# Kernel optimization log

Hardware: AMD Instinct MI355X
Metric: run time of the kernel (lower is better)

The kernel has to match this reference:

```python
import jax, jax.numpy as jnp
import numpy as np
import math

B, N, L, ED, H = 2, 32, 4, 64, 4   # graphs, nodes/graph, layers, embed_dim, heads
HD = ED // H
EPS = 1e-5


def _ln(x, g, b):
    m = x.mean(-1, keepdims=True)
    v = ((x - m) ** 2).mean(-1, keepdims=True)
    return (x - m) * jax.lax.rsqrt(v + EPS) * g + b


def _layer(x, W, b, lg, lb, fW, fb, fg, fbeta):
    # NOTE: in the torch source, ModuleList([Linear]*4) shares ONE linear for
    # q/k/v1/v2 and ONE LayerNorm for norms[0..2]; we reproduce that sharing.
    h = (x @ W.T + b).reshape(B, N, N, H, HD)
    q = _ln(h, lg, lb)                                    # q == k (shared LN)
    scores = jnp.einsum('bxahd,bayhd->bxayh', q, q) / math.sqrt(HD)
    att = jax.nn.softmax(scores, axis=2)                  # softmax over 'a'
    xu = jnp.einsum('bxahd,bayhd->bxayhd', h, h)          # v1 == v2 == h
    xu = _ln(xu, lg, lb)                                  # shared LN again
    xu = jnp.einsum('bxayh,bxayhd->bxyhd', att, xu).reshape(B, N, N, ED)
    y = jnp.concatenate([x, xu], axis=-1) @ fW.T + fb
    return _ln(y, fg, fbeta)


def _diag_offdiag_maxpool(x):
    # x: (B, ED, N, N)
    diag = jnp.diagonal(x, axis1=-2, axis2=-1)            # (B, ED, N)
    max_diag = diag.max(axis=2)                           # (B, ED)
    val = jnp.abs(max_diag.max() + (-x).max())
    eye = jnp.eye(N, dtype=x.dtype)
    max_offdiag = (x - val * eye).max(axis=(2, 3))        # (B, ED)
    return jnp.concatenate([max_diag, max_offdiag], axis=1)  # (B, 2*ED)


def setup_inputs() -> dict:
    key = jax.random.key(0)
    ks = jax.random.split(key, 12)
    E = 1024
    g = jax.random.randint(ks[0], (E,), 0, B)
    ls = jax.random.randint(ks[1], (E,), 0, N)
    ld = jax.random.randint(ks[2], (E,), 0, N)
    edge_index = jnp.stack([g * N + ls, g * N + ld]).astype(jnp.int64)
    batch = (jnp.arange(B * N) // N).astype(jnp.int64)
    std = 0.02
    return {
        'edge_index': edge_index,
        'batch': batch,
        'W0': jax.random.normal(ks[3], (ED, 1), jnp.float32) * std,
        'b0': jnp.zeros((ED,), jnp.float32),
        'Ws': jax.random.normal(ks[4], (L - 1, ED, ED), jnp.float32) * std,
        'bs': jnp.zeros((L - 1, ED), jnp.float32),
        'ln_g': jnp.ones((L, HD), jnp.float32),
        'ln_b': jnp.zeros((L, HD), jnp.float32),
        'fW0': jax.random.normal(ks[5], (ED, 1 + ED), jnp.float32) * std,
        'fb0': jnp.zeros((ED,), jnp.float32),
        'fWs': jax.random.normal(ks[6], (L - 1, ED, 2 * ED), jnp.float32) * std,
        'fbs': jnp.zeros((L - 1, ED), jnp.float32),
        'fln_g': jnp.ones((L, ED), jnp.float32),
        'fln_b': jnp.zeros((L, ED), jnp.float32),
        'opW': jax.random.normal(ks[7], (L, ED // 2, 2 * ED), jnp.float32) * std,
        'opb': jnp.zeros((L, ED // 2), jnp.float32),
    }


def reference(edge_index, batch, W0, b0, Ws, bs, ln_g, ln_b,
              fW0, fb0, fWs, fbs, fln_g, fln_b, opW, opb):
    # to_dense_adj with edge_attr = 1.0
    g = batch[edge_index[0]]
    ls = edge_index[0] - g * N
    ld = edge_index[1] - g * N
    adj = jnp.zeros((B, N, N), jnp.float32).at[g, ls, ld].add(1.0)
    idx = jnp.arange(N)
    adj = adj.at[:, idx, idx].set(2.0)
    x = adj[..., None]                                    # (B, N, N, 1)

    scores = jnp.zeros((B, ED // 2), jnp.float32)
    for i in range(L):
        W = W0 if i == 0 else Ws[i - 1]
        b = b0 if i == 0 else bs[i - 1]
        fW = fW0 if i == 0 else fWs[i - 1]
        fb = fb0 if i == 0 else fbs[i - 1]
        x = _layer(x, W, b, ln_g[i], ln_b[i], fW, fb, fln_g[i], fln_b[i])
        pooled = _diag_offdiag_maxpool(jnp.transpose(x, (0, 3, 1, 2)))
        scores = scores + pooled @ opW[i].T + opb[i]

    # BatchNorm1d(momentum=1.0, affine=False), training mode -> batch stats
    m = scores.mean(axis=0)
    v = scores.var(axis=0)
    return (scores - m) / jnp.sqrt(v + EPS)
```

## Files before the change

### kernel.cpp

```cpp
#include <hip/hip_runtime.h>
#include <math.h>

#define EPS 1e-5f

#define AG_LOAD(p)     __hip_atomic_load((p), __ATOMIC_RELAXED, __HIP_MEMORY_SCOPE_AGENT)
#define AG_STORE(p, v) __hip_atomic_store((p), (v), __ATOMIC_RELAXED, __HIP_MEMORY_SCOPE_AGENT)

struct Params {
    const int* ei; const int* batch; int E;
    const float* W0; const float* b0; const float* Ws; const float* bs;
    const float* ln_g; const float* ln_b;
    const float* fW0; const float* fb0; const float* fWs; const float* fbs;
    const float* fln_g; const float* fln_b;
    const float* opW; const float* opb;
    float* hA; float* qA;
    float* hB; float* qB;
    float* xbuf;
    float* Pmin; float* Poff; float* Pdg;
    int* bar;
    float* out;
};


__launch_bounds__(512, 1)
__global__ void k0(Params p) {
    const int tid  = threadIdx.x;
    const int blk  = blockIdx.x;
    const int gtid = blk * 512 + tid;
    const int c    = tid & 63;
    const int d    = c & 15;
    const int rl   = tid >> 6;
    const int r0     = blk * 8;
    const int b_blk  = r0 >> 10;
    const int xi_blk = (r0 >> 5) & 31;
    const int y0     = r0 & 31;
    const int rld    = xi_blk - y0;
    const int a_l  = c & 31;
    const int h1   = c >> 5;

    __shared__ float xslab[32];
    __shared__ float yslab[256];
    __shared__ __align__(16) float cA[64], cC[64], cW[64], cB0[64], cG[64], cBl[64];
    __shared__ float hstat[3][4];
    __shared__ __align__(16) float pp_s[256 * 68];
    __shared__ float A1_s[8 * 132];
    __shared__ float K0h_s[8][4];
    __shared__ __align__(16) float xrow[8][64];
    __shared__ __align__(16) float xu_s[8][64];
    __shared__ float Wf0[64];
    __shared__ __align__(16) float T65[64 * 68];
    __shared__ __align__(16) float ST[64 * 68];

    if (blk == 0 && tid == 0) p.bar[0] = 0;

    if (tid < 32)  xslab[tid] = 0.0f;
    if (tid < 256) yslab[tid] = 0.0f;

    if (tid < 64) {
        float Wc = p.W0[c], bc = p.b0[c];
        float sW = Wc, sB = bc;
        #pragma unroll
        for (int m = 1; m < 16; m <<= 1) {
            sW += __shfl_xor(sW, m, 16);
            sB += __shfl_xor(sB, m, 16);
        }
        float Ac = Wc - sW * 0.0625f;
        float Bc = bc - sB * 0.0625f;
        float sAA = Ac * Ac, sAB = Ac * Bc, sBB = Bc * Bc;
        #pragma unroll
        for (int m = 1; m < 16; m <<= 1) {
            sAA += __shfl_xor(sAA, m, 16);
            sAB += __shfl_xor(sAB, m, 16);
            sBB += __shfl_xor(sBB, m, 16);
        }
        cA[c] = Ac; cC[c] = Bc; cW[c] = Wc; cB0[c] = bc;
        cG[c] = p.ln_g[d]; cBl[c] = p.ln_b[d];
        if (d == 0) {
            hstat[0][c >> 4] = sAA * 0.0625f;
            hstat[1][c >> 4] = sAB * 0.0625f;
            hstat[2][c >> 4] = sBB * 0.0625f;
        }
        Wf0[tid] = p.fW0[tid * 65];
    }
    for (int i = tid; i < 1024; i += 512) {
        int cc = i >> 4, u = i & 15;
        const float* src = p.fW0 + cc * 65 + 1 + 4 * u;
        float4 w = make_float4(src[0], src[1], src[2], src[3]);
        *(float4*)(T65 + cc * 68 + 4 * ((u + 2 * cc) & 15)) = w;
    }
    for (int i = tid; i < 1024; i += 512) {
        float4 w = ((const float4*)p.Ws)[i];
        int cc = i >> 4, u = i & 15;
        *(float4*)(ST + cc * 68 + 4 * ((u + 2 * cc) & 15)) = w;
    }
    __syncthreads();

    for (int e2 = tid; e2 < p.E; e2 += 512) {
        int e0 = p.ei[e2], e1 = p.ei[p.E + e2];
        int g  = p.batch[e0];
        if (g == b_blk) {
            int ls = e0 - g * 32, ld = e1 - g * 32;
            if (ls == xi_blk) atomicAdd(&xslab[ld], 1.0f);
            unsigned dy = (unsigned)(ld - y0);
            if (dy < 8u) atomicAdd(&yslab[ls * 8 + dy], 1.0f);
        }
    }
    __syncthreads();
    if (tid == 0) xslab[xi_blk] = 2.0f;
    if (tid < 8)  yslab[(y0 + tid) * 8 + tid] = 2.0f;
    __syncthreads();

    const float vx = xslab[a_l];
    const float vy = yslab[a_l * 8 + rl];
    float s0, s1, is0, is1, w0m, w1m;
    {
        const int hh = h1;
        float rsx = rsqrtf(fmaf(fmaf(hstat[0][hh], vx, 2.0f * hstat[1][hh]), vx, hstat[2][hh]) + EPS);
        float rsy = rsqrtf(fmaf(fmaf(hstat[0][hh], vy, 2.0f * hstat[1][hh]), vy, hstat[2][hh]) + EPS);
        float qq = 0.f, sp = 0.f, sq = 0.f;
        #pragma unroll
        for (int t = 0; t < 4; ++t) {
            int dd = hh * 16 + 4 * t;
            float4 av = *(const float4*)(cA + dd);
            float4 bv = *(const float4*)(cC + dd);
            float4 wv = *(const float4*)(cW + dd);
            float4 b0v = *(const float4*)(cB0 + dd);
            float4 gv = *(const float4*)(cG + dd);
            float4 blv = *(const float4*)(cBl + dd);
            float4 ppv;
            float qx, qy;
            qx = fmaf(av.x, vx, bv.x) * rsx * gv.x + blv.x;
            qy = fmaf(av.x, vy, bv.x) * rsy * gv.x + blv.x;
            qq = fmaf(qx, qy, qq);
            ppv.x = fmaf(wv.x, vx, b0v.x) * fmaf(wv.x, vy, b0v.x);
            qx = fmaf(av.y, vx, bv.y) * rsx * gv.y + blv.y;
            qy = fmaf(av.y, vy, bv.y) * rsy * gv.y + blv.y;
            qq = fmaf(qx, qy, qq);
            ppv.y = fmaf(wv.y, vx, b0v.y) * fmaf(wv.y, vy, b0v.y);
            qx = fmaf(av.z, vx, bv.z) * rsx * gv.z + blv.z;
            qy = fmaf(av.z, vy, bv.z) * rsy * gv.z + blv.z;
            qq = fmaf(qx, qy, qq);
            ppv.z = fmaf(wv.z, vx, b0v.z) * fmaf(wv.z, vy, b0v.z);
            qx = fmaf(av.w, vx, bv.w) * rsx * gv.w + blv.w;
            qy = fmaf(av.w, vy, bv.w) * rsy * gv.w + blv.w;
            qq = fmaf(qx, qy, qq);
            ppv.w = fmaf(wv.w, vx, b0v.w) * fmaf(wv.w, vy, b0v.w);
            sp += ppv.x + ppv.y + ppv.z + ppv.w;
            sq += ppv.x*ppv.x + ppv.y*ppv.y + ppv.z*ppv.z + ppv.w*ppv.w;
            *(float4*)(pp_s + (a_l * 8 + rl) * 68 + 4 * (((hh * 4 + t) + 3 * a_l) & 15)) = ppv;
        }
        s0 = qq * 0.25f;
        float mu = sp * 0.0625f, var = fmaxf(sq * 0.0625f - mu * mu, 0.f);
        is0 = rsqrtf(var + EPS); w0m = mu * is0;
    }
    {
        const int hh = h1 + 2;
        float rsx = rsqrtf(fmaf(fmaf(hstat[0][hh], vx, 2.0f * hstat[1][hh]), vx, hstat[2][hh]) + EPS);
        float rsy = rsqrtf(fmaf(fmaf(hstat[0][hh], vy, 2.0f * hstat[1][hh]), vy, hstat[2][hh]) + EPS);
        float qq = 0.f, sp = 0.f, sq = 0.f;
        #pragma unroll
        for (int t = 0; t < 4; ++t) {
            int dd = hh * 16 + 4 * t;
            float4 av = *(const float4*)(cA + dd);
            float4 bv = *(const float4*)(cC + dd);
            float4 wv = *(const float4*)(cW + dd);
            float4 b0v = *(const float4*)(cB0 + dd);
            float4 gv = *(const float4*)(cG + dd);
            float4 blv = *(const float4*)(cBl + dd);
            float4 ppv;
            float qx, qy;
            qx = fmaf(av.x, vx, bv.x) * rsx * gv.x + blv.x;
            qy = fmaf(av.x, vy, bv.x) * rsy * gv.x + blv.x;
            qq = fmaf(qx, qy, qq);
            ppv.x = fmaf(wv.x, vx, b0v.x) * fmaf(wv.x, vy, b0v.x);
            qx = fmaf(av.y, vx, bv.y) * rsx * gv.y + blv.y;
            qy = fmaf(av.y, vy, bv.y) * rsy * gv.y + blv.y;
            qq = fmaf(qx, qy, qq);
            ppv.y = fmaf(wv.y, vx, b0v.y) * fmaf(wv.y, vy, b0v.y);
            qx = fmaf(av.z, vx, bv.z) * rsx * gv.z + blv.z;
            qy = fmaf(av.z, vy, bv.z) * rsy * gv.z + blv.z;
            qq = fmaf(qx, qy, qq);
            ppv.z = fmaf(wv.z, vx, b0v.z) * fmaf(wv.z, vy, b0v.z);
            qx = fmaf(av.w, vx, bv.w) * rsx * gv.w + blv.w;
            qy = fmaf(av.w, vy, bv.w) * rsy * gv.w + blv.w;
            qq = fmaf(qx, qy, qq);
            ppv.w = fmaf(wv.w, vx, b0v.w) * fmaf(wv.w, vy, b0v.w);
            sp += ppv.x + ppv.y + ppv.z + ppv.w;
            sq += ppv.x*ppv.x + ppv.y*ppv.y + ppv.z*ppv.z + ppv.w*ppv.w;
            *(float4*)(pp_s + (a_l * 8 + rl) * 68 + 4 * (((hh * 4 + t) + 3 * a_l) & 15)) = ppv;
        }
        s1 = qq * 0.25f;
        float mu = sp * 0.0625f, var = fmaxf(sq * 0.0625f - mu * mu, 0.f);
        is1 = rsqrtf(var + EPS); w1m = mu * is1;
    }

    float m0 = s0, m1 = s1;
    #pragma unroll
    for (int m = 1; m < 32; m <<= 1) {
        m0 = fmaxf(m0, __shfl_xor(m0, m));
        m1 = fmaxf(m1, __shfl_xor(m1, m));
    }
    float e0 = __expf(s0 - m0), e1 = __expf(s1 - m1);
    float l0 = e0, l1 = e1, k0a = e0 * w0m, k1a = e1 * w1m;
    #pragma unroll
    for (int m = 1; m < 32; m <<= 1) {
        l0 += __shfl_xor(l0, m);  l1 += __shfl_xor(l1, m);
        k0a += __shfl_xor(k0a, m); k1a += __shfl_xor(k1a, m);
    }
    A1_s[rl * 132 + h1 * 33 + a_l]       = e0 * is0 / l0;
    A1_s[rl * 132 + (h1 + 2) * 33 + a_l] = e1 * is1 / l1;
    if (a_l == 0) {
        K0h_s[rl][h1]     = k0a / l0;
        K0h_s[rl][h1 + 2] = k1a / l1;
    }

    {
        const int hc = c >> 4;
        float acc = 0.f;
        #pragma unroll
        for (int a = 0; a < 32; ++a) {
            float pv = pp_s[(a * 8 + rl) * 68 + 4 * (((c >> 2) + 3 * a) & 15) + (c & 3)];
            acc = fmaf(A1_s[rl * 132 + hc * 33 + a], pv, acc);
        }
        xu_s[rl][c] = (acc - K0h_s[rl][hc]) * cG[c] + cBl[c];
    }

    const float adjv = xslab[y0 + rl];
    float acc2 = fmaf(Wf0[c], adjv, p.fb0[c]);
    #pragma unroll
    for (int u = 0; u < 16; ++u) {
        float4 w = *(const float4*)(T65 + c * 68 + 4 * ((u + 2 * c) & 15));
        float4 xr = *(const float4*)(&xu_s[rl][4 * u]);
        acc2 = fmaf(w.x, xr.x, acc2); acc2 = fmaf(w.y, xr.y, acc2);
        acc2 = fmaf(w.z, xr.z, acc2); acc2 = fmaf(w.w, xr.w, acc2);
    }
    float t1 = acc2;
    #pragma unroll
    for (int m = 1; m < 64; m <<= 1) t1 += __shfl_xor(t1, m, 64);
    float mu = t1 * (1.0f / 64.0f);
    float dv2 = acc2 - mu;
    float t2 = dv2 * dv2;
    #pragma unroll
    for (int m = 1; m < 64; m <<= 1) t2 += __shfl_xor(t2, m, 64);
    float xnew = dv2 * rsqrtf(t2 * (1.0f / 64.0f) + EPS) * p.fln_g[c] + p.fln_b[c];
    xrow[rl][c]  = xnew;
    p.xbuf[gtid] = xnew;
    __syncthreads();

    if (tid < 64) {
        float mn = 1e30f, off = -1e30f, dg = -1e30f;
        #pragma unroll
        for (int r2 = 0; r2 < 8; ++r2) {
            float v = xrow[r2][tid];
            mn = fminf(mn, v);
            if (r2 == rld) dg = v; else off = fmaxf(off, v);
        }
        int o = blk * 64 + tid;
        p.Pmin[o] = mn; p.Poff[o] = off; p.Pdg[o] = dg;
    }

    {
        float acc = p.bs[c];
        #pragma unroll
        for (int u = 0; u < 16; ++u) {
            float4 w = *(const float4*)(ST + c * 68 + 4 * ((u + 2 * c) & 15));
            float4 xr = *(const float4*)(&xrow[rl][4 * u]);
            acc = fmaf(w.x, xr.x, acc); acc = fmaf(w.y, xr.y, acc);
            acc = fmaf(w.z, xr.z, acc); acc = fmaf(w.w, xr.w, acc);
        }
        p.hA[gtid] = acc;
        float s1a = acc;
        #pragma unroll
        for (int m = 1; m < 16; m <<= 1) s1a += __shfl_xor(s1a, m, 16);
        float mean = s1a * 0.0625f;
        float dv = acc - mean;
        float s2 = dv * dv;
        #pragma unroll
        for (int m = 1; m < 16; m <<= 1) s2 += __shfl_xor(s2, m, 16);
        p.qA[gtid] = dv * rsqrtf(s2 * 0.0625f + EPS) * p.ln_g[16 + d] + p.ln_b[16 + d];
    }
}

__launch_bounds__(512, 1)
__global__ void klayer(Params p, int layer, int is_last) {
    const int tid  = threadIdx.x;
    const int blk  = blockIdx.x;
    const int gtid = blk * 512 + tid;
    const int c    = tid & 63;
    const int d    = c & 15;
    const int rl   = tid >> 6;
    const int r0     = blk * 8;
    const int b_blk  = r0 >> 10;
    const int xi_blk = (r0 >> 5) & 31;
    const int y0     = r0 & 31;
    const int rld    = xi_blk - y0;
    const int slab_off = (b_blk * 1024 + xi_blk * 32) * 64;
    const int a_l  = c & 31;
    const int h1   = c >> 5;

    const float* hin = (layer == 2) ? p.hB : p.hA;
    const float* qin = (layer == 2) ? p.qB : p.qA;
    float* hout = (layer == 1) ? p.hB : p.hA;
    float* qout = (layer == 1) ? p.qB : p.qA;

    __shared__ __align__(16) float qx_s[32 * 68];
    __shared__ __align__(16) float hx_s[32 * 68];
    __shared__ __align__(16) float pp_s[256 * 68];
    __shared__ float A1_s[8 * 132];
    __shared__ float K0h_s[8][4];
    __shared__ __align__(16) float xrow[8][64];
    __shared__ __align__(16) float xu_s[8][64];
    __shared__ __align__(16) float FT[64 * 132];
    __shared__ __align__(16) float ST[64 * 68];
    __shared__ float vals[4];
    __shared__ float scores_s[64];
    __shared__ int tailflag;
    float* sm_mn  = pp_s;
    float* sm_off = pp_s + 512;
    float* sm_dg  = pp_s + 1024;
    float* psum   = pp_s + 1536;

    float xv = p.xbuf[gtid];
    float4 qsl = ((const float4*)(qin + slab_off))[tid];
    float4 hsl = ((const float4*)(hin + slab_off))[tid];
    const float* qyp = qin + (b_blk * 1024 + a_l * 32 + y0 + rl) * 64;
    const float* hyp = hin + (b_blk * 1024 + a_l * 32 + y0 + rl) * 64;
    float4 qvA[4], hvA[4], qvB[4], hvB[4];
    #pragma unroll
    for (int t = 0; t < 4; ++t) {
        qvA[t] = *(const float4*)(qyp + h1 * 16 + 4 * t);
        hvA[t] = *(const float4*)(hyp + h1 * 16 + 4 * t);
        qvB[t] = *(const float4*)(qyp + (h1 + 2) * 16 + 4 * t);
        hvB[t] = *(const float4*)(hyp + (h1 + 2) * 16 + 4 * t);
    }
    const float gl = p.ln_g[layer * 16 + d], bl = p.ln_b[layer * 16 + d];

    {
        int a = tid >> 4, t = tid & 15, pr = (t + 2 * a) & 15;
        *(float4*)(qx_s + a * 68 + 4 * pr) = qsl;
        *(float4*)(hx_s + a * 68 + 4 * pr) = hsl;
    }
    {
        const float* fw = p.fWs + (layer - 1) * 8192;
        for (int i = tid; i < 2048; i += 512) {
            float4 w = ((const float4*)fw)[i];
            int cc = i >> 5, u = i & 31;
            *(float4*)(FT + cc * 132 + 4 * ((u + 2 * cc) & 31)) = w;
        }
    }
    if (!is_last) {
        const float* sw = p.Ws + layer * 4096;
        for (int i = tid; i < 1024; i += 512) {
            float4 w = ((const float4*)sw)[i];
            int cc = i >> 4, u = i & 15;
            *(float4*)(ST + cc * 68 + 4 * ((u + 2 * cc) & 15)) = w;
        }
    }
    xrow[rl][c] = xv;
    __syncthreads();

    float s0, s1, is0, is1, w0m, w1m;
    {
        const int hh = h1;
        float qq = 0.f, sp = 0.f, sq = 0.f;
        #pragma unroll
        for (int t = 0; t < 4; ++t) {
            float4 xq = *(const float4*)(qx_s + a_l * 68 + 4 * (((hh * 4 + t) + 2 * a_l) & 15));
            float4 xh = *(const float4*)(hx_s + a_l * 68 + 4 * (((hh * 4 + t) + 2 * a_l) & 15));
            float4 yq = qvA[t], yh = hvA[t];
            float4 ppv;
            ppv.x = xh.x * yh.x; ppv.y = xh.y * yh.y;
            ppv.z = xh.z * yh.z; ppv.w = xh.w * yh.w;
            qq = fmaf(xq.x, yq.x, qq); qq = fmaf(xq.y, yq.y, qq);
            qq = fmaf(xq.z, yq.z, qq); qq = fmaf(xq.w, yq.w, qq);
            sp += ppv.x + ppv.y + ppv.z + ppv.w;
            sq += ppv.x*ppv.x + ppv.y*ppv.y + ppv.z*ppv.z + ppv.w*ppv.w;
            *(float4*)(pp_s + (a_l * 8 + rl) * 68 + 4 * (((hh * 4 + t) + 3 * a_l) & 15)) = ppv;
        }
        s0 = qq * 0.25f;
        float mu = sp * 0.0625f, var = fmaxf(sq * 0.0625f - mu * mu, 0.f);
        is0 = rsqrtf(var + EPS); w0m = mu * is0;
    }
    {
        const int hh = h1 + 2;
        float qq = 0.f, sp = 0.f, sq = 0.f;
        #pragma unroll
        for (int t = 0; t < 4; ++t) {
            float4 xq = *(const float4*)(qx_s + a_l * 68 + 4 * (((hh * 4 + t) + 2 * a_l) & 15));
            float4 xh = *(const float4*)(hx_s + a_l * 68 + 4 * (((hh * 4 + t) + 2 * a_l) & 15));
            float4 yq = qvB[t], yh = hvB[t];
            float4 ppv;
            ppv.x = xh.x * yh.x; ppv.y = xh.y * yh.y;
            ppv.z = xh.z * yh.z; ppv.w = xh.w * yh.w;
            qq = fmaf(xq.x, yq.x, qq); qq = fmaf(xq.y, yq.y, qq);
            qq = fmaf(xq.z, yq.z, qq); qq = fmaf(xq.w, yq.w, qq);
            sp += ppv.x + ppv.y + ppv.z + ppv.w;
            sq += ppv.x*ppv.x + ppv.y*ppv.y + ppv.z*ppv.z + ppv.w*ppv.w;
            *(float4*)(pp_s + (a_l * 8 + rl) * 68 + 4 * (((hh * 4 + t) + 3 * a_l) & 15)) = ppv;
        }
        s1 = qq * 0.25f;
        float mu = sp * 0.0625f, var = fmaxf(sq * 0.0625f - mu * mu, 0.f);
        is1 = rsqrtf(var + EPS); w1m = mu * is1;
    }

    float m0 = s0, m1 = s1;
    #pragma unroll
    for (int m = 1; m < 32; m <<= 1) {
        m0 = fmaxf(m0, __shfl_xor(m0, m));
        m1 = fmaxf(m1, __shfl_xor(m1, m));
    }
    float e0 = __expf(s0 - m0), e1 = __expf(s1 - m1);
    float l0 = e0, l1 = e1, k0a = e0 * w0m, k1a = e1 * w1m;
    #pragma unroll
    for (int m = 1; m < 32; m <<= 1) {
        l0 += __shfl_xor(l0, m);  l1 += __shfl_xor(l1, m);
        k0a += __shfl_xor(k0a, m); k1a += __shfl_xor(k1a, m);
    }
    A1_s[rl * 132 + h1 * 33 + a_l]       = e0 * is0 / l0;
    A1_s[rl * 132 + (h1 + 2) * 33 + a_l] = e1 * is1 / l1;
    if (a_l == 0) {
        K0h_s[rl][h1]     = k0a / l0;
        K0h_s[rl][h1 + 2] = k1a / l1;
    }

    {
        const int hc = c >> 4;
        float acc = 0.f;
        #pragma unroll
        for (int a = 0; a < 32; ++a) {
            float pv = pp_s[(a * 8 + rl) * 68 + 4 * (((c >> 2) + 3 * a) & 15) + (c & 3)];
            acc = fmaf(A1_s[rl * 132 + hc * 33 + a], pv, acc);
        }
        xu_s[rl][c] = (acc - K0h_s[rl][hc]) * gl + bl;
    }

    float acc2 = p.fbs[(layer - 1) * 64 + c];
    #pragma unroll
    for (int u = 0; u < 16; ++u) {
        float4 w = *(const float4*)(FT + c * 132 + 4 * ((u + 2 * c) & 31));
        float4 xr = *(const float4*)(&xrow[rl][4 * u]);
        acc2 = fmaf(w.x, xr.x, acc2); acc2 = fmaf(w.y, xr.y, acc2);
        acc2 = fmaf(w.z, xr.z, acc2); acc2 = fmaf(w.w, xr.w, acc2);
    }
    #pragma unroll
    for (int u = 16; u < 32; ++u) {
        float4 w = *(const float4*)(FT + c * 132 + 4 * ((u + 2 * c) & 31));
        float4 xr = *(const float4*)(&xu_s[rl][4 * (u - 16)]);
        acc2 = fmaf(w.x, xr.x, acc2); acc2 = fmaf(w.y, xr.y, acc2);
        acc2 = fmaf(w.z, xr.z, acc2); acc2 = fmaf(w.w, xr.w, acc2);
    }
    float t1 = acc2;
    #pragma unroll
    for (int m = 1; m < 64; m <<= 1) t1 += __shfl_xor(t1, m, 64);
    float mu = t1 * (1.0f / 64.0f);
    float dv2 = acc2 - mu;
    float t2 = dv2 * dv2;
    #pragma unroll
    for (int m = 1; m < 64; m <<= 1) t2 += __shfl_xor(t2, m, 64);
    float xnew = dv2 * rsqrtf(t2 * (1.0f / 64.0f) + EPS) *
                 p.fln_g[layer * 64 + c] + p.fln_b[layer * 64 + c];
    __syncthreads();
    xrow[rl][c] = xnew;
    if (!is_last) p.xbuf[gtid] = xnew;
    __syncthreads();

    if (tid < 64) {
        float mn = 1e30f, off = -1e30f, dg = -1e30f;
        #pragma unroll
        for (int r2 = 0; r2 < 8; ++r2) {
            float v = xrow[r2][tid];
            mn = fminf(mn, v);
            if (r2 == rld) dg = v; else off = fmaxf(off, v);
        }
        int o = layer * 16384 + blk * 64 + tid;
        if (is_last) {
            AG_STORE(&p.Pmin[o], mn); AG_STORE(&p.Poff[o], off); AG_STORE(&p.Pdg[o], dg);
        } else {
            p.Pmin[o] = mn; p.Poff[o] = off; p.Pdg[o] = dg;
        }
    }

    if (!is_last) {
        float acc = p.bs[layer * 64 + c];
        #pragma unroll
        for (int u = 0; u < 16; ++u) {
            float4 w = *(const float4*)(ST + c * 68 + 4 * ((u + 2 * c) & 15));
            float4 xr = *(const float4*)(&xrow[rl][4 * u]);
            acc = fmaf(w.x, xr.x, acc); acc = fmaf(w.y, xr.y, acc);
            acc = fmaf(w.z, xr.z, acc); acc = fmaf(w.w, xr.w, acc);
        }
        hout[gtid] = acc;
        float s1a = acc;
        #pragma unroll
        for (int m = 1; m < 16; m <<= 1) s1a += __shfl_xor(s1a, m, 16);
        float mean = s1a * 0.0625f;
        float dv = acc - mean;
        float s2 = dv * dv;
        #pragma unroll
        for (int m = 1; m < 16; m <<= 1) s2 += __shfl_xor(s2, m, 16);
        qout[gtid] = dv * rsqrtf(s2 * 0.0625f + EPS) *
                     p.ln_g[(layer + 1) * 16 + d] + p.ln_b[(layer + 1) * 16 + d];
        return;
    }

    __syncthreads();
    if (tid == 0) {
        int r = __hip_atomic_fetch_add(p.bar, 1, __ATOMIC_RELAXED,
                                       __HIP_MEMORY_SCOPE_AGENT);
        tailflag = (r == 255) ? 1 : 0;
    }
    __syncthreads();
    if (!tailflag) return;

    {
        int l = tid >> 7, bb = (tid >> 6) & 1, e = tid & 63;
        float mn = 1e30f, off = -1e30f, dg = -1e30f;
        #pragma unroll 4
        for (int k = 0; k < 128; ++k) {
            int o = l * 16384 + (bb * 128 + k) * 64 + e;
            float vmn, voff, vdg;
            if (l == 3) { vmn = AG_LOAD(&p.Pmin[o]); voff = AG_LOAD(&p.Poff[o]); vdg = AG_LOAD(&p.Pdg[o]); }
            else        { vmn = p.Pmin[o];           voff = p.Poff[o];           vdg = p.Pdg[o]; }
            mn  = fminf(mn,  vmn);
            off = fmaxf(off, voff);
            dg  = fmaxf(dg,  vdg);
        }
        sm_mn[tid] = mn; sm_off[tid] = off; sm_dg[tid] = dg;
    }
    __syncthreads();
    if (tid < 4) {
        float gmx = -1e30f, gmn = 1e30f;
        for (int i2 = 0; i2 < 128; ++i2) {
            gmx = fmaxf(gmx, sm_dg[tid * 128 + i2]);
            gmn = fminf(gmn, sm_mn[tid * 128 + i2]);
        }
        vals[tid] = fabsf(gmx - gmn);
    }
    __syncthreads();
    {
        int bb = tid >> 8, cc = (tid >> 3) & 31, pp = tid & 7;
        float a2 = 0.0f;
        for (int l = 0; l < 4; ++l) {
            float val = vals[l];
            const float* Wr = p.opW + l * 4096 + cc * 128;
            int base = l * 128 + bb * 64;
            for (int j = pp * 16; j < pp * 16 + 16; ++j) {
                float pv;
                if (j < 64) pv = sm_dg[base + j];
                else        pv = fmaxf(sm_off[base + j - 64], sm_dg[base + j - 64] - val);
                a2 = fmaf(Wr[j], pv, a2);
            }
        }
        psum[tid] = a2;
    }
    __syncthreads();
    if (tid < 64) {
        int bb = tid >> 5, cc = tid & 31;
        float a2 = 0.0f;
        for (int l = 0; l < 4; ++l) a2 += p.opb[l * 32 + cc];
        for (int pp = 0; pp < 8; ++pp) a2 += psum[bb * 256 + cc * 8 + pp];
        scores_s[tid] = a2;
    }
    __syncthreads();
    if (tid < 32) {
        float sA = scores_s[tid], sB = scores_s[32 + tid];
        float mu2 = 0.5f * (sA + sB);
        float va = 0.5f * ((sA - mu2) * (sA - mu2) + (sB - mu2) * (sB - mu2));
        float inv = rsqrtf(va + EPS);
        p.out[tid]      = (sA - mu2) * inv;
        p.out[32 + tid] = (sB - mu2) * inv;
    }
}

extern "C" void kernel_launch(void* const* d_in, const int* in_sizes, int n_in,
                              void* d_out, int out_size, void* d_ws, size_t ws_size,
                              hipStream_t stream) {
    Params prm;
    prm.ei    = (const int*)d_in[0];
    prm.batch = (const int*)d_in[1];
    prm.E     = in_sizes[0] / 2;
    prm.W0    = (const float*)d_in[2];
    prm.b0    = (const float*)d_in[3];
    prm.Ws    = (const float*)d_in[4];
    prm.bs    = (const float*)d_in[5];
    prm.ln_g  = (const float*)d_in[6];
    prm.ln_b  = (const float*)d_in[7];
    prm.fW0   = (const float*)d_in[8];
    prm.fb0   = (const float*)d_in[9];
    prm.fWs   = (const float*)d_in[10];
    prm.fbs   = (const float*)d_in[11];
    prm.fln_g = (const float*)d_in[12];
    prm.fln_b = (const float*)d_in[13];
    prm.opW   = (const float*)d_in[14];
    prm.opb   = (const float*)d_in[15];

    float* ws = (float*)d_ws;
    prm.hA    = ws;
    prm.qA    = prm.hA   + 131072;
    prm.hB    = prm.qA   + 131072;
    prm.qB    = prm.hB   + 131072;
    prm.xbuf  = prm.qB   + 131072;
    prm.Pmin  = prm.xbuf + 131072;
    prm.Poff  = prm.Pmin + 65536;
    prm.Pdg   = prm.Poff + 65536;
    prm.bar   = (int*)(prm.Pdg + 65536);
    prm.out   = (float*)d_out;

    k0<<<256, 512, 0, stream>>>(prm);
    klayer<<<256, 512, 0, stream>>>(prm, 1, 0);
    klayer<<<256, 512, 0, stream>>>(prm, 2, 0);
    klayer<<<256, 512, 0, stream>>>(prm, 3, 1);
}
```

Before: 162.8 us.

## Fuse four layer kernels into one persistent kernel with grid barriers

Merges the initial layer kernel and the three per-layer kernels into one persistent kernel with 256 blocks. Blocks synchronise between layers through an atomic-counter grid barrier instead of separate launches. The final pooling and batch-norm tail runs on block 0 after a last barrier, and a memset clears the barrier counters before launch. This removes launch gaps between the four stages, but relies on all 256 blocks being co-resident and adds spin-wait barrier cost.

```diff
diff --git a/kernel.cpp b/kernel.cpp
--- a/kernel.cpp
+++ b/kernel.cpp
@@ -21,268 +21,23 @@
     float* out;
 };
 
+__device__ __forceinline__ void gridbar(int* bar, int ph) {
+    __syncthreads();
+    __threadfence();
+    if (threadIdx.x == 0) {
+        int r = atomicAdd(&bar[ph], 1);
+        if (r == 255) {
+            AG_STORE(&bar[8 + ph], 1);
+        } else {
+            while (AG_LOAD(&bar[8 + ph]) == 0) __builtin_amdgcn_s_sleep(8);
+        }
+    }
+    __syncthreads();
+    __threadfence();
+}
 
 __launch_bounds__(512, 1)
-__global__ void k0(Params p) {
-    const int tid  = threadIdx.x;
-    const int blk  = blockIdx.x;
-    const int gtid = blk * 512 + tid;
-    const int c    = tid & 63;
-    const int d    = c & 15;
-    const int rl   = tid >> 6;
-    const int r0     = blk * 8;
-    const int b_blk  = r0 >> 10;
-    const int xi_blk = (r0 >> 5) & 31;
-    const int y0     = r0 & 31;
-    const int rld    = xi_blk - y0;
-    const int a_l  = c & 31;
-    const int h1   = c >> 5;
-
-    __shared__ float xslab[32];
-    __shared__ float yslab[256];
-    __shared__ __align__(16) float cA[64], cC[64], cW[64], cB0[64], cG[64], cBl[64];
-    __shared__ float hstat[3][4];
-    __shared__ __align__(16) float pp_s[256 * 68];
-    __shared__ float A1_s[8 * 132];
-    __shared__ float K0h_s[8][4];
-    __shared__ __align__(16) float xrow[8][64];
-    __shared__ __align__(16) float xu_s[8][64];
-    __shared__ float Wf0[64];
-    __shared__ __align__(16) float T65[64 * 68];
-    __shared__ __align__(16) float ST[64 * 68];
-
-    if (blk == 0 && tid == 0) p.bar[0] = 0;
-
-    if (tid < 32)  xslab[tid] = 0.0f;
-    if (tid < 256) yslab[tid] = 0.0f;
-
-    if (tid < 64) {
-        float Wc = p.W0[c], bc = p.b0[c];
-        float sW = Wc, sB = bc;
-        #pragma unroll
-        for (int m = 1; m < 16; m <<= 1) {
-            sW += __shfl_xor(sW, m, 16);
-            sB += __shfl_xor(sB, m, 16);
-        }
-        float Ac = Wc - sW * 0.0625f;
-        float Bc = bc - sB * 0.0625f;
-        float sAA = Ac * Ac, sAB = Ac * Bc, sBB = Bc * Bc;
-        #pragma unroll
-        for (int m = 1; m < 16; m <<= 1) {
-            sAA += __shfl_xor(sAA, m, 16);
-            sAB += __shfl_xor(sAB, m, 16);
-            sBB += __shfl_xor(sBB, m, 16);
-        }
-        cA[c] = Ac; cC[c] = Bc; cW[c] = Wc; cB0[c] = bc;
-        cG[c] = p.ln_g[d]; cBl[c] = p.ln_b[d];
-        if (d == 0) {
-            hstat[0][c >> 4] = sAA * 0.0625f;
-            hstat[1][c >> 4] = sAB * 0.0625f;
-            hstat[2][c >> 4] = sBB * 0.0625f;
-        }
-        Wf0[tid] = p.fW0[tid * 65];
-    }
-    for (int i = tid; i < 1024; i += 512) {
-        int cc = i >> 4, u = i & 15;
-        const float* src = p.fW0 + cc * 65 + 1 + 4 * u;
-        float4 w = make_float4(src[0], src[1], src[2], src[3]);
-        *(float4*)(T65 + cc * 68 + 4 * ((u + 2 * cc) & 15)) = w;
-    }
-    for (int i = tid; i < 1024; i += 512) {
-        float4 w = ((const float4*)p.Ws)[i];
-        int cc = i >> 4, u = i & 15;
-        *(float4*)(ST + cc * 68 + 4 * ((u + 2 * cc) & 15)) = w;
-    }
-    __syncthreads();
-
-    for (int e2 = tid; e2 < p.E; e2 += 512) {
-        int e0 = p.ei[e2], e1 = p.ei[p.E + e2];
-        int g  = p.batch[e0];
-        if (g == b_blk) {
-            int ls = e0 - g * 32, ld = e1 - g * 32;
-            if (ls == xi_blk) atomicAdd(&xslab[ld], 1.0f);
-            unsigned dy = (unsigned)(ld - y0);
-            if (dy < 8u) atomicAdd(&yslab[ls * 8 + dy], 1.0f);
-        }
-    }
-    __syncthreads();
-    if (tid == 0) xslab[xi_blk] = 2.0f;
-    if (tid < 8)  yslab[(y0 + tid) * 8 + tid] = 2.0f;
-    __syncthreads();
-
-    const float vx = xslab[a_l];
-    const float vy = yslab[a_l * 8 + rl];
-    float s0, s1, is0, is1, w0m, w1m;
-    {
-        const int hh = h1;
-        float rsx = rsqrtf(fmaf(fmaf(hstat[0][hh], vx, 2.0f * hstat[1][hh]), vx, hstat[2][hh]) + EPS);
-        float rsy = rsqrtf(fmaf(fmaf(hstat[0][hh], vy, 2.0f * hstat[1][hh]), vy, hstat[2][hh]) + EPS);
-        float qq = 0.f, sp = 0.f, sq = 0.f;
-        #pragma unroll
-        for (int t = 0; t < 4; ++t) {
-            int dd = hh * 16 + 4 * t;
-            float4 av = *(const float4*)(cA + dd);
-            float4 bv = *(const float4*)(cC + dd);
-            float4 wv = *(const float4*)(cW + dd);
-            float4 b0v = *(const float4*)(cB0 + dd);
-            float4 gv = *(const float4*)(cG + dd);
-            float4 blv = *(const float4*)(cBl + dd);
-            float4 ppv;
-            float qx, qy;
-            qx = fmaf(av.x, vx, bv.x) * rsx * gv.x + blv.x;
-            qy = fmaf(av.x, vy, bv.x) * rsy * gv.x + blv.x;
-            qq = fmaf(qx, qy, qq);
-            ppv.x = fmaf(wv.x, vx, b0v.x) * fmaf(wv.x, vy, b0v.x);
-            qx = fmaf(av.y, vx, bv.y) * rsx * gv.y + blv.y;
-            qy = fmaf(av.y, vy, bv.y) * rsy * gv.y + blv.y;
-            qq = fmaf(qx, qy, qq);
-            ppv.y = fmaf(wv.y, vx, b0v.y) * fmaf(wv.y, vy, b0v.y);
-            qx = fmaf(av.z, vx, bv.z) * rsx * gv.z + blv.z;
-            qy = fmaf(av.z, vy, bv.z) * rsy * gv.z + blv.z;
-            qq = fmaf(qx, qy, qq);
-            ppv.z = fmaf(wv.z, vx, b0v.z) * fmaf(wv.z, vy, b0v.z);
-            qx = fmaf(av.w, vx, bv.w) * rsx * gv.w + blv.w;
-            qy = fmaf(av.w, vy, bv.w) * rsy * gv.w + blv.w;
-            qq = fmaf(qx, qy, qq);
-            ppv.w = fmaf(wv.w, vx, b0v.w) * fmaf(wv.w, vy, b0v.w);
-            sp += ppv.x + ppv.y + ppv.z + ppv.w;
-            sq += ppv.x*ppv.x + ppv.y*ppv.y + ppv.z*ppv.z + ppv.w*ppv.w;
-            *(float4*)(pp_s + (a_l * 8 + rl) * 68 + 4 * (((hh * 4 + t) + 3 * a_l) & 15)) = ppv;
-        }
-        s0 = qq * 0.25f;
-        float mu = sp * 0.0625f, var = fmaxf(sq * 0.0625f - mu * mu, 0.f);
-        is0 = rsqrtf(var + EPS); w0m = mu * is0;
-    }
-    {
-        const int hh = h1 + 2;
-        float rsx = rsqrtf(fmaf(fmaf(hstat[0][hh], vx, 2.0f * hstat[1][hh]), vx, hstat[2][hh]) + EPS);
-        float rsy = rsqrtf(fmaf(fmaf(hstat[0][hh], vy, 2.0f * hstat[1][hh]), vy, hstat[2][hh]) + EPS);
-        float qq = 0.f, sp = 0.f, sq = 0.f;
-        #pragma unroll
-        for (int t = 0; t < 4; ++t) {
-            int dd = hh * 16 + 4 * t;
-            float4 av = *(const float4*)(cA + dd);
-            float4 bv = *(const float4*)(cC + dd);
-            float4 wv = *(const float4*)(cW + dd);
-            float4 b0v = *(const float4*)(cB0 + dd);
-            float4 gv = *(const float4*)(cG + dd);
-            float4 blv = *(const float4*)(cBl + dd);
-            float4 ppv;
-            float qx, qy;
-            qx = fmaf(av.x, vx, bv.x) * rsx * gv.x + blv.x;
-            qy = fmaf(av.x, vy, bv.x) * rsy * gv.x + blv.x;
-            qq = fmaf(qx, qy, qq);
-            ppv.x = fmaf(wv.x, vx, b0v.x) * fmaf(wv.x, vy, b0v.x);
-            qx = fmaf(av.y, vx, bv.y) * rsx * gv.y + blv.y;
-            qy = fmaf(av.y, vy, bv.y) * rsy * gv.y + blv.y;
-            qq = fmaf(qx, qy, qq);
-            ppv.y = fmaf(wv.y, vx, b0v.y) * fmaf(wv.y, vy, b0v.y);
-            qx = fmaf(av.z, vx, bv.z) * rsx * gv.z + blv.z;
-            qy = fmaf(av.z, vy, bv.z) * rsy * gv.z + blv.z;
-            qq = fmaf(qx, qy, qq);
-            ppv.z = fmaf(wv.z, vx, b0v.z) * fmaf(wv.z, vy, b0v.z);
-            qx = fmaf(av.w, vx, bv.w) * rsx * gv.w + blv.w;
-            qy = fmaf(av.w, vy, bv.w) * rsy * gv.w + blv.w;
-            qq = fmaf(qx, qy, qq);
-            ppv.w = fmaf(wv.w, vx, b0v.w) * fmaf(wv.w, vy, b0v.w);
-            sp += ppv.x + ppv.y + ppv.z + ppv.w;
-            sq += ppv.x*ppv.x + ppv.y*ppv.y + ppv.z*ppv.z + ppv.w*ppv.w;
-            *(float4*)(pp_s + (a_l * 8 + rl) * 68 + 4 * (((hh * 4 + t) + 3 * a_l) & 15)) = ppv;
-        }
-        s1 = qq * 0.25f;
-        float mu = sp * 0.0625f, var = fmaxf(sq * 0.0625f - mu * mu, 0.f);
-        is1 = rsqrtf(var + EPS); w1m = mu * is1;
-    }
-
-    float m0 = s0, m1 = s1;
-    #pragma unroll
-    for (int m = 1; m < 32; m <<= 1) {
-        m0 = fmaxf(m0, __shfl_xor(m0, m));
-        m1 = fmaxf(m1, __shfl_xor(m1, m));
-    }
-    float e0 = __expf(s0 - m0), e1 = __expf(s1 - m1);
-    float l0 = e0, l1 = e1, k0a = e0 * w0m, k1a = e1 * w1m;
-    #pragma unroll
-    for (int m = 1; m < 32; m <<= 1) {
-        l0 += __shfl_xor(l0, m);  l1 += __shfl_xor(l1, m);
-        k0a += __shfl_xor(k0a, m); k1a += __shfl_xor(k1a, m);
-    }
-    A1_s[rl * 132 + h1 * 33 + a_l]       = e0 * is0 / l0;
-    A1_s[rl * 132 + (h1 + 2) * 33 + a_l] = e1 * is1 / l1;
-    if (a_l == 0) {
-        K0h_s[rl][h1]     = k0a / l0;
-        K0h_s[rl][h1 + 2] = k1a / l1;
-    }
-
-    {
-        const int hc = c >> 4;
-        float acc = 0.f;
-        #pragma unroll
-        for (int a = 0; a < 32; ++a) {
-            float pv = pp_s[(a * 8 + rl) * 68 + 4 * (((c >> 2) + 3 * a) & 15) + (c & 3)];
-            acc = fmaf(A1_s[rl * 132 + hc * 33 + a], pv, acc);
-        }
-        xu_s[rl][c] = (acc - K0h_s[rl][hc]) * cG[c] + cBl[c];
-    }
-
-    const float adjv = xslab[y0 + rl];
-    float acc2 = fmaf(Wf0[c], adjv, p.fb0[c]);
-    #pragma unroll
-    for (int u = 0; u < 16; ++u) {
-        float4 w = *(const float4*)(T65 + c * 68 + 4 * ((u + 2 * c) & 15));
-        float4 xr = *(const float4*)(&xu_s[rl][4 * u]);
-        acc2 = fmaf(w.x, xr.x, acc2); acc2 = fmaf(w.y, xr.y, acc2);
-        acc2 = fmaf(w.z, xr.z, acc2); acc2 = fmaf(w.w, xr.w, acc2);
-    }
-    float t1 = acc2;
-    #pragma unroll
-    for (int m = 1; m < 64; m <<= 1) t1 += __shfl_xor(t1, m, 64);
-    float mu = t1 * (1.0f / 64.0f);
-    float dv2 = acc2 - mu;
-    float t2 = dv2 * dv2;
-    #pragma unroll
-    for (int m = 1; m < 64; m <<= 1) t2 += __shfl_xor(t2, m, 64);
-    float xnew = dv2 * rsqrtf(t2 * (1.0f / 64.0f) + EPS) * p.fln_g[c] + p.fln_b[c];
-    xrow[rl][c]  = xnew;
-    p.xbuf[gtid] = xnew;
-    __syncthreads();
-
-    if (tid < 64) {
-        float mn = 1e30f, off = -1e30f, dg = -1e30f;
-        #pragma unroll
-        for (int r2 = 0; r2 < 8; ++r2) {
-            float v = xrow[r2][tid];
-            mn = fminf(mn, v);
-            if (r2 == rld) dg = v; else off = fmaxf(off, v);
-        }
-        int o = blk * 64 + tid;
-        p.Pmin[o] = mn; p.Poff[o] = off; p.Pdg[o] = dg;
-    }
-
-    {
-        float acc = p.bs[c];
-        #pragma unroll
-        for (int u = 0; u < 16; ++u) {
-            float4 w = *(const float4*)(ST + c * 68 + 4 * ((u + 2 * c) & 15));
-            float4 xr = *(const float4*)(&xrow[rl][4 * u]);
-            acc = fmaf(w.x, xr.x, acc); acc = fmaf(w.y, xr.y, acc);
-            acc = fmaf(w.z, xr.z, acc); acc = fmaf(w.w, xr.w, acc);
-        }
-        p.hA[gtid] = acc;
-        float s1a = acc;
-        #pragma unroll
-        for (int m = 1; m < 16; m <<= 1) s1a += __shfl_xor(s1a, m, 16);
-        float mean = s1a * 0.0625f;
-        float dv = acc - mean;
-        float s2 = dv * dv;
-        #pragma unroll
-        for (int m = 1; m < 16; m <<= 1) s2 += __shfl_xor(s2, m, 16);
-        p.qA[gtid] = dv * rsqrtf(s2 * 0.0625f + EPS) * p.ln_g[16 + d] + p.ln_b[16 + d];
-    }
-}
-
-__launch_bounds__(512, 1)
-__global__ void klayer(Params p, int layer, int is_last) {
+__global__ void kfused(Params p) {
     const int tid  = threadIdx.x;
     const int blk  = blockIdx.x;
     const int gtid = blk * 512 + tid;
@@ -298,11 +53,6 @@
     const int a_l  = c & 31;
     const int h1   = c >> 5;
 
-    const float* hin = (layer == 2) ? p.hB : p.hA;
-    const float* qin = (layer == 2) ? p.qB : p.qA;
-    float* hout = (layer == 1) ? p.hB : p.hA;
-    float* qout = (layer == 1) ? p.qB : p.qA;
-
     __shared__ __align__(16) float qx_s[32 * 68];
     __shared__ __align__(16) float hx_s[32 * 68];
     __shared__ __align__(16) float pp_s[256 * 68];
@@ -314,203 +64,433 @@
     __shared__ __align__(16) float ST[64 * 68];
     __shared__ float vals[4];
     __shared__ float scores_s[64];
-    __shared__ int tailflag;
+    __shared__ float xslab[32];
+    __shared__ float yslab[256];
+    __shared__ __align__(16) float cA[64], cC[64], cW[64], cB0[64], cG[64], cBl[64];
+    __shared__ float hstat[3][4];
+    __shared__ float Wf0[64];
+
+    float* T65 = FT;
     float* sm_mn  = pp_s;
     float* sm_off = pp_s + 512;
     float* sm_dg  = pp_s + 1024;
     float* psum   = pp_s + 1536;
 
-    float xv = p.xbuf[gtid];
-    float4 qsl = ((const float4*)(qin + slab_off))[tid];
-    float4 hsl = ((const float4*)(hin + slab_off))[tid];
-    const float* qyp = qin + (b_blk * 1024 + a_l * 32 + y0 + rl) * 64;
-    const float* hyp = hin + (b_blk * 1024 + a_l * 32 + y0 + rl) * 64;
-    float4 qvA[4], hvA[4], qvB[4], hvB[4];
-    #pragma unroll
-    for (int t = 0; t < 4; ++t) {
-        qvA[t] = *(const float4*)(qyp + h1 * 16 + 4 * t);
-        hvA[t] = *(const float4*)(hyp + h1 * 16 + 4 * t);
-        qvB[t] = *(const float4*)(qyp + (h1 + 2) * 16 + 4 * t);
-        hvB[t] = *(const float4*)(hyp + (h1 + 2) * 16 + 4 * t);
-    }
-    const float gl = p.ln_g[layer * 16 + d], bl = p.ln_b[layer * 16 + d];
-
     {
-        int a = tid >> 4, t = tid & 15, pr = (t + 2 * a) & 15;
-        *(float4*)(qx_s + a * 68 + 4 * pr) = qsl;
-        *(float4*)(hx_s + a * 68 + 4 * pr) = hsl;
-    }
-    {
-        const float* fw = p.fWs + (layer - 1) * 8192;
-        for (int i = tid; i < 2048; i += 512) {
-            float4 w = ((const float4*)fw)[i];
-            int cc = i >> 5, u = i & 31;
-            *(float4*)(FT + cc * 132 + 4 * ((u + 2 * cc) & 31)) = w;
-        }
-    }
-    if (!is_last) {
-        const float* sw = p.Ws + layer * 4096;
+        if (tid < 32)  xslab[tid] = 0.0f;
+        if (tid < 256) yslab[tid] = 0.0f;
+
+        if (tid < 64) {
+            float Wc = p.W0[c], bc = p.b0[c];
+            float sW = Wc, sB = bc;
+            #pragma unroll
+            for (int m = 1; m < 16; m <<= 1) {
+                sW += __shfl_xor(sW, m, 16);
+                sB += __shfl_xor(sB, m, 16);
+            }
+            float Ac = Wc - sW * 0.0625f;
+            float Bc = bc - sB * 0.0625f;
+            float sAA = Ac * Ac, sAB = Ac * Bc, sBB = Bc * Bc;
+            #pragma unroll
+            for (int m = 1; m < 16; m <<= 1) {
+                sAA += __shfl_xor(sAA, m, 16);
+                sAB += __shfl_xor(sAB, m, 16);
+                sBB += __shfl_xor(sBB, m, 16);
+            }
+            cA[c] = Ac; cC[c] = Bc; cW[c] = Wc; cB0[c] = bc;
+            cG[c] = p.ln_g[d]; cBl[c] = p.ln_b[d];
+            if (d == 0) {
+                hstat[0][c >> 4] = sAA * 0.0625f;
+                hstat[1][c >> 4] = sAB * 0.0625f;
+                hstat[2][c >> 4] = sBB * 0.0625f;
+            }
+            Wf0[tid] = p.fW0[tid * 65];
+        }
         for (int i = tid; i < 1024; i += 512) {
-            float4 w = ((const float4*)sw)[i];
+            int cc = i >> 4, u = i & 15;
+            const float* src = p.fW0 + cc * 65 + 1 + 4 * u;
+            float4 w = make_float4(src[0], src[1], src[2], src[3]);
+            *(float4*)(T65 + cc * 68 + 4 * ((u + 2 * cc) & 15)) = w;
+        }
+        for (int i = tid; i < 1024; i += 512) {
+            float4 w = ((const float4*)p.Ws)[i];
             int cc = i >> 4, u = i & 15;
             *(float4*)(ST + cc * 68 + 4 * ((u + 2 * cc) & 15)) = w;
         }
-    }
-    xrow[rl][c] = xv;
-    __syncthreads();
-
-    float s0, s1, is0, is1, w0m, w1m;
-    {
-        const int hh = h1;
-        float qq = 0.f, sp = 0.f, sq = 0.f;
+        __syncthreads();
+
+        for (int e2 = tid; e2 < p.E; e2 += 512) {
+            int e0 = p.ei[e2], e1 = p.ei[p.E + e2];
+            int g  = p.batch[e0];
+            if (g == b_blk) {
+                int ls = e0 - g * 32, ld = e1 - g * 32;
+                if (ls == xi_blk) atomicAdd(&xslab[ld], 1.0f);
+                unsigned dy = (unsigned)(ld - y0);
+                if (dy < 8u) atomicAdd(&yslab[ls * 8 + dy], 1.0f);
+            }
+        }
+        __syncthreads();
+        if (tid == 0) xslab[xi_blk] = 2.0f;
+        if (tid < 8)  yslab[(y0 + tid) * 8 + tid] = 2.0f;
+        __syncthreads();
+
+        const float vx = xslab[a_l];
+        const float vy = yslab[a_l * 8 + rl];
+        float s0, s1, is0, is1, w0m, w1m;
+        {
+            const int hh = h1;
+            float rsx = rsqrtf(fmaf(fmaf(hstat[0][hh], vx, 2.0f * hstat[1][hh]), vx, hstat[2][hh]) + EPS);
+            float rsy = rsqrtf(fmaf(fmaf(hstat[0][hh], vy, 2.0f * hstat[1][hh]), vy, hstat[2][hh]) + EPS);
+            float qq = 0.f, sp = 0.f, sq = 0.f;
+            #pragma unroll
+            for (int t = 0; t < 4; ++t) {
+                int dd = hh * 16 + 4 * t;
+                float4 av = *(const float4*)(cA + dd);
+                float4 bv = *(const float4*)(cC + dd);
+                float4 wv = *(const float4*)(cW + dd);
+                float4 b0v = *(const float4*)(cB0 + dd);
+                float4 gv = *(const float4*)(cG + dd);
+                float4 blv = *(const float4*)(cBl + dd);
+                float4 ppv;
+                float qx, qy;
+                qx = fmaf(av.x, vx, bv.x) * rsx * gv.x + blv.x;
+                qy = fmaf(av.x, vy, bv.x) * rsy * gv.x + blv.x;
+                qq = fmaf(qx, qy, qq);
+                ppv.x = fmaf(wv.x, vx, b0v.x) * fmaf(wv.x, vy, b0v.x);
+                qx = fmaf(av.y, vx, bv.y) * rsx * gv.y + blv.y;
+                qy = fmaf(av.y, vy, bv.y) * rsy * gv.y + blv.y;
+                qq = fmaf(qx, qy, qq);
+                ppv.y = fmaf(wv.y, vx, b0v.y) * fmaf(wv.y, vy, b0v.y);
+                qx = fmaf(av.z, vx, bv.z) * rsx * gv.z + blv.z;
+                qy = fmaf(av.z, vy, bv.z) * rsy * gv.z + blv.z;
+                qq = fmaf(qx, qy, qq);
+                ppv.z = fmaf(wv.z, vx, b0v.z) * fmaf(wv.z, vy, b0v.z);
+                qx = fmaf(av.w, vx, bv.w) * rsx * gv.w + blv.w;
+                qy = fmaf(av.w, vy, bv.w) * rsy * gv.w + blv.w;
+                qq = fmaf(qx, qy, qq);
+                ppv.w = fmaf(wv.w, vx, b0v.w) * fmaf(wv.w, vy, b0v.w);
+                sp += ppv.x + ppv.y + ppv.z + ppv.w;
+                sq += ppv.x*ppv.x + ppv.y*ppv.y + ppv.z*ppv.z + ppv.w*ppv.w;
+                *(float4*)(pp_s + (a_l * 8 + rl) * 68 + 4 * (((hh * 4 + t) + 3 * a_l) & 15)) = ppv;
+            }
+            s0 = qq * 0.25f;
+            float mu = sp * 0.0625f, var = fmaxf(sq * 0.0625f - mu * mu, 0.f);
+            is0 = rsqrtf(var + EPS); w0m = mu * is0;
+        }
+        {
+            const int hh = h1 + 2;
+            float rsx = rsqrtf(fmaf(fmaf(hstat[0][hh], vx, 2.0f * hstat[1][hh]), vx, hstat[2][hh]) + EPS);
+            float rsy = rsqrtf(fmaf(fmaf(hstat[0][hh], vy, 2.0f * hstat[1][hh]), vy, hstat[2][hh]) + EPS);
+            float qq = 0.f, sp = 0.f, sq = 0.f;
+            #pragma unroll
+            for (int t = 0; t < 4; ++t) {
+                int dd = hh * 16 + 4 * t;
+                float4 av = *(const float4*)(cA + dd);
+                float4 bv = *(const float4*)(cC + dd);
+                float4 wv = *(const float4*)(cW + dd);
+                float4 b0v = *(const float4*)(cB0 + dd);
+                float4 gv = *(const float4*)(cG + dd);
+                float4 blv = *(const float4*)(cBl + dd);
+                float4 ppv;
+                float qx, qy;
+                qx = fmaf(av.x, vx, bv.x) * rsx * gv.x + blv.x;
+                qy = fmaf(av.x, vy, bv.x) * rsy * gv.x + blv.x;
+                qq = fmaf(qx, qy, qq);
+                ppv.x = fmaf(wv.x, vx, b0v.x) * fmaf(wv.x, vy, b0v.x);
+                qx = fmaf(av.y, vx, bv.y) * rsx * gv.y + blv.y;
+                qy = fmaf(av.y, vy, bv.y) * rsy * gv.y + blv.y;
+                qq = fmaf(qx, qy, qq);
+                ppv.y = fmaf(wv.y, vx, b0v.y) * fmaf(wv.y, vy, b0v.y);
+                qx = fmaf(av.z, vx, bv.z) * rsx * gv.z + blv.z;
+                qy = fmaf(av.z, vy, bv.z) * rsy * gv.z + blv.z;
+                qq = fmaf(qx, qy, qq);
+                ppv.z = fmaf(wv.z, vx, b0v.z) * fmaf(wv.z, vy, b0v.z);
+                qx = fmaf(av.w, vx, bv.w) * rsx * gv.w + blv.w;
+                qy = fmaf(av.w, vy, bv.w) * rsy * gv.w + blv.w;
+                qq = fmaf(qx, qy, qq);
+                ppv.w = fmaf(wv.w, vx, b0v.w) * fmaf(wv.w, vy, b0v.w);
+                sp += ppv.x + ppv.y + ppv.z + ppv.w;
+                sq += ppv.x*ppv.x + ppv.y*ppv.y + ppv.z*ppv.z + ppv.w*ppv.w;
+                *(float4*)(pp_s + (a_l * 8 + rl) * 68 + 4 * (((hh * 4 + t) + 3 * a_l) & 15)) = ppv;
+            }
+            s1 = qq * 0.25f;
+            float mu = sp * 0.0625f, var = fmaxf(sq * 0.0625f - mu * mu, 0.f);
+            is1 = rsqrtf(var + EPS); w1m = mu * is1;
+        }
+
+        float m0 = s0, m1 = s1;
+        #pragma unroll
+        for (int m = 1; m < 32; m <<= 1) {
+            m0 = fmaxf(m0, __shfl_xor(m0, m));
+            m1 = fmaxf(m1, __shfl_xor(m1, m));
+        }
+        float e0 = __expf(s0 - m0), e1 = __expf(s1 - m1);
+        float l0 = e0, l1 = e1, k0a = e0 * w0m, k1a = e1 * w1m;
+        #pragma unroll
+        for (int m = 1; m < 32; m <<= 1) {
+            l0 += __shfl_xor(l0, m);  l1 += __shfl_xor(l1, m);
+            k0a += __shfl_xor(k0a, m); k1a += __shfl_xor(k1a, m);
+        }
+        A1_s[rl * 132 + h1 * 33 + a_l]       = e0 * is0 / l0;
+        A1_s[rl * 132 + (h1 + 2) * 33 + a_l] = e1 * is1 / l1;
+        if (a_l == 0) {
+            K0h_s[rl][h1]     = k0a / l0;
+            K0h_s[rl][h1 + 2] = k1a / l1;
+        }
+
+        {
+            const int hc = c >> 4;
+            float acc = 0.f;
+            #pragma unroll
+            for (int a = 0; a < 32; ++a) {
+                float pv = pp_s[(a * 8 + rl) * 68 + 4 * (((c >> 2) + 3 * a) & 15) + (c & 3)];
+                acc = fmaf(A1_s[rl * 132 + hc * 33 + a], pv, acc);
+            }
+            xu_s[rl][c] = (acc - K0h_s[rl][hc]) * cG[c] + cBl[c];
+        }
+
+        const float adjv = xslab[y0 + rl];
+        float acc2 = fmaf(Wf0[c], adjv, p.fb0[c]);
+        #pragma unroll
+        for (int u = 0; u < 16; ++u) {
+            float4 w = *(const float4*)(T65 + c * 68 + 4 * ((u + 2 * c) & 15));
+            float4 xr = *(const float4*)(&xu_s[rl][4 * u]);
+            acc2 = fmaf(w.x, xr.x, acc2); acc2 = fmaf(w.y, xr.y, acc2);
+            acc2 = fmaf(w.z, xr.z, acc2); acc2 = fmaf(w.w, xr.w, acc2);
+        }
+        float t1 = acc2;
+        #pragma unroll
+        for (int m = 1; m < 64; m <<= 1) t1 += __shfl_xor(t1, m, 64);
+        float mu = t1 * (1.0f / 64.0f);
+        float dv2 = acc2 - mu;
+        float t2 = dv2 * dv2;
+        #pragma unroll
+        for (int m = 1; m < 64; m <<= 1) t2 += __shfl_xor(t2, m, 64);
+        float xnew = dv2 * rsqrtf(t2 * (1.0f / 64.0f) + EPS) * p.fln_g[c] + p.fln_b[c];
+        xrow[rl][c] = xnew;
+        __syncthreads();
+
+        if (tid < 64) {
+            float mn = 1e30f, off = -1e30f, dg = -1e30f;
+            #pragma unroll
+            for (int r2 = 0; r2 < 8; ++r2) {
+                float v = xrow[r2][tid];
+                mn = fminf(mn, v);
+                if (r2 == rld) dg = v; else off = fmaxf(off, v);
+            }
+            int o = blk * 64 + tid;
+            p.Pmin[o] = mn; p.Poff[o] = off; p.Pdg[o] = dg;
+        }
+
+        {
+            float acc = p.bs[c];
+            #pragma unroll
+            for (int u = 0; u < 16; ++u) {
+                float4 w = *(const float4*)(ST + c * 68 + 4 * ((u + 2 * c) & 15));
+                float4 xr = *(const float4*)(&xrow[rl][4 * u]);
+                acc = fmaf(w.x, xr.x, acc); acc = fmaf(w.y, xr.y, acc);
+                acc = fmaf(w.z, xr.z, acc); acc = fmaf(w.w, xr.w, acc);
+            }
+            p.hA[gtid] = acc;
+            float s1a = acc;
+            #pragma unroll
+            for (int m = 1; m < 16; m <<= 1) s1a += __shfl_xor(s1a, m, 16);
+            float mean = s1a * 0.0625f;
+            float dv = acc - mean;
+            float s2 = dv * dv;
+            #pragma unroll
+            for (int m = 1; m < 16; m <<= 1) s2 += __shfl_xor(s2, m, 16);
+            p.qA[gtid] = dv * rsqrtf(s2 * 0.0625f + EPS) * p.ln_g[16 + d] + p.ln_b[16 + d];
+        }
+    }
+    gridbar(p.bar, 0);
+
+    #pragma unroll 1
+    for (int layer = 1; layer <= 3; ++layer) {
+        const float* hin = (layer == 2) ? p.hB : p.hA;
+        const float* qin = (layer == 2) ? p.qB : p.qA;
+        float* hout = (layer == 1) ? p.hB : p.hA;
+        float* qout = (layer == 1) ? p.qB : p.qA;
+
+        float4 qsl = ((const float4*)(qin + slab_off))[tid];
+        float4 hsl = ((const float4*)(hin + slab_off))[tid];
+        const float* qyp = qin + (b_blk * 1024 + a_l * 32 + y0 + rl) * 64;
+        const float* hyp = hin + (b_blk * 1024 + a_l * 32 + y0 + rl) * 64;
+        float4 qvA[4], hvA[4], qvB[4], hvB[4];
         #pragma unroll
         for (int t = 0; t < 4; ++t) {
-            float4 xq = *(const float4*)(qx_s + a_l * 68 + 4 * (((hh * 4 + t) + 2 * a_l) & 15));
-            float4 xh = *(const float4*)(hx_s + a_l * 68 + 4 * (((hh * 4 + t) + 2 * a_l) & 15));
-            float4 yq = qvA[t], yh = hvA[t];
-            float4 ppv;
-            ppv.x = xh.x * yh.x; ppv.y = xh.y * yh.y;
-            ppv.z = xh.z * yh.z; ppv.w = xh.w * yh.w;
-            qq = fmaf(xq.x, yq.x, qq); qq = fmaf(xq.y, yq.y, qq);
-            qq = fmaf(xq.z, yq.z, qq); qq = fmaf(xq.w, yq.w, qq);
-            sp += ppv.x + ppv.y + ppv.z + ppv.w;
-            sq += ppv.x*ppv.x + ppv.y*ppv.y + ppv.z*ppv.z + ppv.w*ppv.w;
-            *(float4*)(pp_s + (a_l * 8 + rl) * 68 + 4 * (((hh * 4 + t) + 3 * a_l) & 15)) = ppv;
-        }
-        s0 = qq * 0.25f;
-        float mu = sp * 0.0625f, var = fmaxf(sq * 0.0625f - mu * mu, 0.f);
-        is0 = rsqrtf(var + EPS); w0m = mu * is0;
-    }
-    {
-        const int hh = h1 + 2;
-        float qq = 0.f, sp = 0.f, sq = 0.f;
-        #pragma unroll
-        for (int t = 0; t < 4; ++t) {
-            float4 xq = *(const float4*)(qx_s + a_l * 68 + 4 * (((hh * 4 + t) + 2 * a_l) & 15));
-            float4 xh = *(const float4*)(hx_s + a_l * 68 + 4 * (((hh * 4 + t) + 2 * a_l) & 15));
-            float4 yq = qvB[t], yh = hvB[t];
-            float4 ppv;
-            ppv.x = xh.x * yh.x; ppv.y = xh.y * yh.y;
-            ppv.z = xh.z * yh.z; ppv.w = xh.w * yh.w;
-            qq = fmaf(xq.x, yq.x, qq); qq = fmaf(xq.y, yq.y, qq);
-            qq = fmaf(xq.z, yq.z, qq); qq = fmaf(xq.w, yq.w, qq);
-            sp += ppv.x + ppv.y + ppv.z + ppv.w;
-            sq += ppv.x*ppv.x + ppv.y*ppv.y + ppv.z*ppv.z + ppv.w*ppv.w;
-            *(float4*)(pp_s + (a_l * 8 + rl) * 68 + 4 * (((hh * 4 + t) + 3 * a_l) & 15)) = ppv;
-        }
-        s1 = qq * 0.25f;
-        float mu = sp * 0.0625f, var = fmaxf(sq * 0.0625f - mu * mu, 0.f);
-        is1 = rsqrtf(var + EPS); w1m = mu * is1;
-    }
-
-    float m0 = s0, m1 = s1;
-    #pragma unroll
-    for (int m = 1; m < 32; m <<= 1) {
-        m0 = fmaxf(m0, __shfl_xor(m0, m));
-        m1 = fmaxf(m1, __shfl_xor(m1, m));
-    }
-    float e0 = __expf(s0 - m0), e1 = __expf(s1 - m1);
-    float l0 = e0, l1 = e1, k0a = e0 * w0m, k1a = e1 * w1m;
-    #pragma unroll
-    for (int m = 1; m < 32; m <<= 1) {
-        l0 += __shfl_xor(l0, m);  l1 += __shfl_xor(l1, m);
-        k0a += __shfl_xor(k0a, m); k1a += __shfl_xor(k1a, m);
-    }
-    A1_s[rl * 132 + h1 * 33 + a_l]       = e0 * is0 / l0;
-    A1_s[rl * 132 + (h1 + 2) * 33 + a_l] = e1 * is1 / l1;
-    if (a_l == 0) {
-        K0h_s[rl][h1]     = k0a / l0;
-        K0h_s[rl][h1 + 2] = k1a / l1;
-    }
-
-    {
-        const int hc = c >> 4;
-        float acc = 0.f;
-        #pragma unroll
-        for (int a = 0; a < 32; ++a) {
-            float pv = pp_s[(a * 8 + rl) * 68 + 4 * (((c >> 2) + 3 * a) & 15) + (c & 3)];
-            acc = fmaf(A1_s[rl * 132 + hc * 33 + a], pv, acc);
-        }
-        xu_s[rl][c] = (acc - K0h_s[rl][hc]) * gl + bl;
-    }
-
-    float acc2 = p.fbs[(layer - 1) * 64 + c];
-    #pragma unroll
-    for (int u = 0; u < 16; ++u) {
-        float4 w = *(const float4*)(FT + c * 132 + 4 * ((u + 2 * c) & 31));
-        float4 xr = *(const float4*)(&xrow[rl][4 * u]);
-        acc2 = fmaf(w.x, xr.x, acc2); acc2 = fmaf(w.y, xr.y, acc2);
-        acc2 = fmaf(w.z, xr.z, acc2); acc2 = fmaf(w.w, xr.w, acc2);
-    }
-    #pragma unroll
-    for (int u = 16; u < 32; ++u) {
-        float4 w = *(const float4*)(FT + c * 132 + 4 * ((u + 2 * c) & 31));
-        float4 xr = *(const float4*)(&xu_s[rl][4 * (u - 16)]);
-        acc2 = fmaf(w.x, xr.x, acc2); acc2 = fmaf(w.y, xr.y, acc2);
-        acc2 = fmaf(w.z, xr.z, acc2); acc2 = fmaf(w.w, xr.w, acc2);
-    }
-    float t1 = acc2;
-    #pragma unroll
-    for (int m = 1; m < 64; m <<= 1) t1 += __shfl_xor(t1, m, 64);
-    float mu = t1 * (1.0f / 64.0f);
-    float dv2 = acc2 - mu;
-    float t2 = dv2 * dv2;
-    #pragma unroll
-    for (int m = 1; m < 64; m <<= 1) t2 += __shfl_xor(t2, m, 64);
-    float xnew = dv2 * rsqrtf(t2 * (1.0f / 64.0f) + EPS) *
-                 p.fln_g[layer * 64 + c] + p.fln_b[layer * 64 + c];
-    __syncthreads();
-    xrow[rl][c] = xnew;
-    if (!is_last) p.xbuf[gtid] = xnew;
-    __syncthreads();
-
-    if (tid < 64) {
-        float mn = 1e30f, off = -1e30f, dg = -1e30f;
-        #pragma unroll
-        for (int r2 = 0; r2 < 8; ++r2) {
-            float v = xrow[r2][tid];
-            mn = fminf(mn, v);
-            if (r2 == rld) dg = v; else off = fmaxf(off, v);
-        }
-        int o = layer * 16384 + blk * 64 + tid;
-        if (is_last) {
-            AG_STORE(&p.Pmin[o], mn); AG_STORE(&p.Poff[o], off); AG_STORE(&p.Pdg[o], dg);
-        } else {
+            qvA[t] = *(const float4*)(qyp + h1 * 16 + 4 * t);
+            hvA[t] = *(const float4*)(hyp + h1 * 16 + 4 * t);
+            qvB[t] = *(const float4*)(qyp + (h1 + 2) * 16 + 4 * t);
+            hvB[t] = *(const float4*)(hyp + (h1 + 2) * 16 + 4 * t);
+        }
+        const float gl = p.ln_g[layer * 16 + d], bl = p.ln_b[layer * 16 + d];
+
+        {
+            int a = tid >> 4, t = tid & 15, pr = (t + 2 * a) & 15;
+            *(float4*)(qx_s + a * 68 + 4 * pr) = qsl;
+            *(float4*)(hx_s + a * 68 + 4 * pr) = hsl;
+        }
+        {
+            const float* fw = p.fWs + (layer - 1) * 8192;
+            for (int i = tid; i < 2048; i += 512) {
+                float4 w = ((const float4*)fw)[i];
+                int cc = i >> 5, u = i & 31;
+                *(float4*)(FT + cc * 132 + 4 * ((u + 2 * cc) & 31)) = w;
+            }
+        }
+        if (layer < 3) {
+            const float* sw = p.Ws + layer * 4096;
+            for (int i = tid; i < 1024; i += 512) {
+                float4 w = ((const float4*)sw)[i];
+                int cc = i >> 4, u = i & 15;
+                *(float4*)(ST + cc * 68 + 4 * ((u + 2 * cc) & 15)) = w;
+            }
+        }
+        __syncthreads();
+
+        float s0, s1, is0, is1, w0m, w1m;
+        {
+            const int hh = h1;
+            float qq = 0.f, sp = 0.f, sq = 0.f;
+            #pragma unroll
+            for (int t = 0; t < 4; ++t) {
+                float4 xq = *(const float4*)(qx_s + a_l * 68 + 4 * (((hh * 4 + t) + 2 * a_l) & 15));
+                float4 xh = *(const float4*)(hx_s + a_l * 68 + 4 * (((hh * 4 + t) + 2 * a_l) & 15));
+                float4 yq = qvA[t], yh = hvA[t];
+                float4 ppv;
+                ppv.x = xh.x * yh.x; ppv.y = xh.y * yh.y;
+                ppv.z = xh.z * yh.z; ppv.w = xh.w * yh.w;
+                qq = fmaf(xq.x, yq.x, qq); qq = fmaf(xq.y, yq.y, qq);
+                qq = fmaf(xq.z, yq.z, qq); qq = fmaf(xq.w, yq.w, qq);
+                sp += ppv.x + ppv.y + ppv.z + ppv.w;
+                sq += ppv.x*ppv.x + ppv.y*ppv.y + ppv.z*ppv.z + ppv.w*ppv.w;
+                *(float4*)(pp_s + (a_l * 8 + rl) * 68 + 4 * (((hh * 4 + t) + 3 * a_l) & 15)) = ppv;
+            }
+            s0 = qq * 0.25f;
+            float mu = sp * 0.0625f, var = fmaxf(sq * 0.0625f - mu * mu, 0.f);
+            is0 = rsqrtf(var + EPS); w0m = mu * is0;
+        }
+        {
+            const int hh = h1 + 2;
+            float qq = 0.f, sp = 0.f, sq = 0.f;
+            #pragma unroll
+            for (int t = 0; t < 4; ++t) {
+                float4 xq = *(const float4*)(qx_s + a_l * 68 + 4 * (((hh * 4 + t) + 2 * a_l) & 15));
+                float4 xh = *(const float4*)(hx_s + a_l * 68 + 4 * (((hh * 4 + t) + 2 * a_l) & 15));
+                float4 yq = qvB[t], yh = hvB[t];
+                float4 ppv;
+                ppv.x = xh.x * yh.x; ppv.y = xh.y * yh.y;
+                ppv.z = xh.z * yh.z; ppv.w = xh.w * yh.w;
+                qq = fmaf(xq.x, yq.x, qq); qq = fmaf(xq.y, yq.y, qq);
+                qq = fmaf(xq.z, yq.z, qq); qq = fmaf(xq.w, yq.w, qq);
+                sp += ppv.x + ppv.y + ppv.z + ppv.w;
+                sq += ppv.x*ppv.x + ppv.y*ppv.y + ppv.z*ppv.z + ppv.w*ppv.w;
+                *(float4*)(pp_s + (a_l * 8 + rl) * 68 + 4 * (((hh * 4 + t) + 3 * a_l) & 15)) = ppv;
+            }
+            s1 = qq * 0.25f;
+            float mu = sp * 0.0625f, var = fmaxf(sq * 0.0625f - mu * mu, 0.f);
+            is1 = rsqrtf(var + EPS); w1m = mu * is1;
+        }
+
+        float m0 = s0, m1 = s1;
+        #pragma unroll
+        for (int m = 1; m < 32; m <<= 1) {
+            m0 = fmaxf(m0, __shfl_xor(m0, m));
+            m1 = fmaxf(m1, __shfl_xor(m1, m));
+        }
+        float e0 = __expf(s0 - m0), e1 = __expf(s1 - m1);
+        float l0 = e0, l1 = e1, k0a = e0 * w0m, k1a = e1 * w1m;
+        #pragma unroll
+        for (int m = 1; m < 32; m <<= 1) {
+            l0 += __shfl_xor(l0, m);  l1 += __shfl_xor(l1, m);
+            k0a += __shfl_xor(k0a, m); k1a += __shfl_xor(k1a, m);
+        }
+        A1_s[rl * 132 + h1 * 33 + a_l]       = e0 * is0 / l0;
+        A1_s[rl * 132 + (h1 + 2) * 33 + a_l] = e1 * is1 / l1;
+        if (a_l == 0) {
+            K0h_s[rl][h1]     = k0a / l0;
+            K0h_s[rl][h1 + 2] = k1a / l1;
+        }
+
+        {
+            const int hc = c >> 4;
+            float acc = 0.f;
+            #pragma unroll
+            for (int a = 0; a < 32; ++a) {
+                float pv = pp_s[(a * 8 + rl) * 68 + 4 * (((c >> 2) + 3 * a) & 15) + (c & 3)];
+                acc = fmaf(A1_s[rl * 132 + hc * 33 + a], pv, acc);
+            }
+            xu_s[rl][c] = (acc - K0h_s[rl][hc]) * gl + bl;
+        }
+
+        float acc2 = p.fbs[(layer - 1) * 64 + c];
+        #pragma unroll
+        for (int u = 0; u < 16; ++u) {
+            float4 w = *(const float4*)(FT + c * 132 + 4 * ((u + 2 * c) & 31));
+            float4 xr = *(const float4*)(&xrow[rl][4 * u]);
+            acc2 = fmaf(w.x, xr.x, acc2); acc2 = fmaf(w.y, xr.y, acc2);
+            acc2 = fmaf(w.z, xr.z, acc2); acc2 = fmaf(w.w, xr.w, acc2);
+        }
+        #pragma unroll
+        for (int u = 16; u < 32; ++u) {
+            float4 w = *(const float4*)(FT + c * 132 + 4 * ((u + 2 * c) & 31));
+            float4 xr = *(const float4*)(&xu_s[rl][4 * (u - 16)]);
+            acc2 = fmaf(w.x, xr.x, acc2); acc2 = fmaf(w.y, xr.y, acc2);
+            acc2 = fmaf(w.z, xr.z, acc2); acc2 = fmaf(w.w, xr.w, acc2);
+        }
+        float t1 = acc2;
+        #pragma unroll
+        for (int m = 1; m < 64; m <<= 1) t1 += __shfl_xor(t1, m, 64);
+        float mu = t1 * (1.0f / 64.0f);
+        float dv2 = acc2 - mu;
+        float t2 = dv2 * dv2;
+        #pragma unroll
+        for (int m = 1; m < 64; m <<= 1) t2 += __shfl_xor(t2, m, 64);
+        float xnew = dv2 * rsqrtf(t2 * (1.0f / 64.0f) + EPS) *
+                     p.fln_g[layer * 64 + c] + p.fln_b[layer * 64 + c];
+        __syncthreads();
+        xrow[rl][c] = xnew;
+        __syncthreads();
+
+        if (tid < 64) {
+            float mn = 1e30f, off = -1e30f, dg = -1e30f;
+            #pragma unroll
+            for (int r2 = 0; r2 < 8; ++r2) {
+                float v = xrow[r2][tid];
+                mn = fminf(mn, v);
+                if (r2 == rld) dg = v; else off = fmaxf(off, v);
+            }
+            int o = layer * 16384 + blk * 64 + tid;
             p.Pmin[o] = mn; p.Poff[o] = off; p.Pdg[o] = dg;
         }
-    }
-
-    if (!is_last) {
-        float acc = p.bs[layer * 64 + c];
-        #pragma unroll
-        for (int u = 0; u < 16; ++u) {
-            float4 w = *(const float4*)(ST + c * 68 + 4 * ((u + 2 * c) & 15));
-            float4 xr = *(const float4*)(&xrow[rl][4 * u]);
-            acc = fmaf(w.x, xr.x, acc); acc = fmaf(w.y, xr.y, acc);
-            acc = fmaf(w.z, xr.z, acc); acc = fmaf(w.w, xr.w, acc);
-        }
-        hout[gtid] = acc;
-        float s1a = acc;
-        #pragma unroll
-        for (int m = 1; m < 16; m <<= 1) s1a += __shfl_xor(s1a, m, 16);
-        float mean = s1a * 0.0625f;
-        float dv = acc - mean;
-        float s2 = dv * dv;
-        #pragma unroll
-        for (int m = 1; m < 16; m <<= 1) s2 += __shfl_xor(s2, m, 16);
-        qout[gtid] = dv * rsqrtf(s2 * 0.0625f + EPS) *
-                     p.ln_g[(layer + 1) * 16 + d] + p.ln_b[(layer + 1) * 16 + d];
-        return;
-    }
-
-    __syncthreads();
-    if (tid == 0) {
-        int r = __hip_atomic_fetch_add(p.bar, 1, __ATOMIC_RELAXED,
-                                       __HIP_MEMORY_SCOPE_AGENT);
-        tailflag = (r == 255) ? 1 : 0;
-    }
-    __syncthreads();
-    if (!tailflag) return;
+
+        if (layer < 3) {
+            float acc = p.bs[layer * 64 + c];
+            #pragma unroll
+            for (int u = 0; u < 16; ++u) {
+                float4 w = *(const float4*)(ST + c * 68 + 4 * ((u + 2 * c) & 15));
+                float4 xr = *(const float4*)(&xrow[rl][4 * u]);
+                acc = fmaf(w.x, xr.x, acc); acc = fmaf(w.y, xr.y, acc);
+                acc = fmaf(w.z, xr.z, acc); acc = fmaf(w.w, xr.w, acc);
+            }
+            hout[gtid] = acc;
+            float s1a = acc;
+            #pragma unroll
+            for (int m = 1; m < 16; m <<= 1) s1a += __shfl_xor(s1a, m, 16);
+            float mean = s1a * 0.0625f;
+            float dv = acc - mean;
+            float s2 = dv * dv;
+            #pragma unroll
+            for (int m = 1; m < 16; m <<= 1) s2 += __shfl_xor(s2, m, 16);
+            qout[gtid] = dv * rsqrtf(s2 * 0.0625f + EPS) *
+                         p.ln_g[(layer + 1) * 16 + d] + p.ln_b[(layer + 1) * 16 + d];
+            gridbar(p.bar, layer);
+        }
+    }
+
+    gridbar(p.bar, 3);
+    if (blk != 0) return;
 
     {
         int l = tid >> 7, bb = (tid >> 6) & 1, e = tid & 63;
@@ -518,12 +498,9 @@
         #pragma unroll 4
         for (int k = 0; k < 128; ++k) {
             int o = l * 16384 + (bb * 128 + k) * 64 + e;
-            float vmn, voff, vdg;
-            if (l == 3) { vmn = AG_LOAD(&p.Pmin[o]); voff = AG_LOAD(&p.Poff[o]); vdg = AG_LOAD(&p.Pdg[o]); }
-            else        { vmn = p.Pmin[o];           voff = p.Poff[o];           vdg = p.Pdg[o]; }
-            mn  = fminf(mn,  vmn);
-            off = fmaxf(off, voff);
-            dg  = fmaxf(dg,  vdg);
+            mn  = fminf(mn,  p.Pmin[o]);
+            off = fmaxf(off, p.Poff[o]);
+            dg  = fmaxf(dg,  p.Pdg[o]);
         }
         sm_mn[tid] = mn; sm_off[tid] = off; sm_dg[tid] = dg;
     }
@@ -606,8 +583,6 @@
     prm.bar   = (int*)(prm.Pdg + 65536);
     prm.out   = (float*)d_out;
 
-    k0<<<256, 512, 0, stream>>>(prm);
-    klayer<<<256, 512, 0, stream>>>(prm, 1, 0);
-    klayer<<<256, 512, 0, stream>>>(prm, 2, 0);
-    klayer<<<256, 512, 0, stream>>>(prm, 3, 1);
+    hipMemsetAsync(prm.bar, 0, 16 * sizeof(int), stream);
+    kfused<<<256, 512, 0, stream>>>(prm);
 }
```

Measured after the change: 393.1 us. +141.4%, slower.
